# Performance work log

Hardware: AMD Instinct MI355X
Metric: run time of the kernel (lower is better)

The kernel has to match this reference:

```python
import jax, jax.numpy as jnp
import numpy as np

WS = 8      # window size
SS = 4      # shift size
NH = 4      # num heads
EPS = 1e-5
MLP_RATIO = 4


def _win_part(x, ws):
    # x: [B,D,H,W,C] -> [B*nD*nH*nW, ws^3, C]
    B, D, H, W, C = x.shape
    x = x.reshape(B, D // ws, ws, H // ws, ws, W // ws, ws, C)
    x = x.transpose(0, 1, 3, 5, 2, 4, 6, 7)
    return x.reshape(-1, ws * ws * ws, C)


def _win_rev(w, ws, B, D, H, W):
    C = w.shape[-1]
    x = w.reshape(B, D // ws, H // ws, W // ws, ws, ws, ws, C)
    x = x.transpose(0, 1, 4, 2, 5, 3, 6, 7)
    return x.reshape(B, D, H, W, C)


def _ln(x, g, b):
    m = jnp.mean(x, axis=-1, keepdims=True)
    v = jnp.mean((x - m) ** 2, axis=-1, keepdims=True)
    return (x - m) / jnp.sqrt(v + EPS) * g + b


def _rel_index(ws):
    coords = np.stack(np.meshgrid(np.arange(ws), np.arange(ws), np.arange(ws), indexing='ij'))  # [3,ws,ws,ws]
    cf = coords.reshape(3, -1)                      # [3, ws^3]
    rel = (cf[:, :, None] - cf[:, None, :]).transpose(1, 2, 0) + (ws - 1)  # [N,N,3]
    return rel[..., 0] * (2 * ws - 1) ** 2 + rel[..., 1] * (2 * ws - 1) + rel[..., 2]


def _attn_mask(D, H, W, ws, ss):
    img = np.zeros((1, D, H, W, 1), dtype=np.float32)
    cnt = 0
    sl = (slice(0, -ws), slice(-ws, -ss), slice(-ss, None))
    for d in sl:
        for h in sl:
            for w in sl:
                img[:, d, h, w, :] = cnt
                cnt += 1
    mw = np.asarray(_win_part(jnp.asarray(img), ws))[..., 0]  # [nW, ws^3]
    diff = mw[:, None, :] - mw[:, :, None]
    return np.where(diff != 0, -100.0, 0.0).astype(np.float32)


def setup_inputs() -> dict:
    key = jax.random.key(0)
    ks = jax.random.split(key, 12)
    B, D, H, W, C = 1, 16, 64, 64, 128
    mh = MLP_RATIO * C
    s = 0.02
    return {
        'x': jax.random.normal(ks[0], (B, D, H, W, C), jnp.float32),
        'attn_mask': jnp.asarray(_attn_mask(D, H, W, WS, SS)),
        'rel_index': jnp.asarray(_rel_index(WS), jnp.int32),
        'rel_bias': jax.random.normal(ks[1], ((2 * WS - 1) ** 3, NH), jnp.float32) * s,
        'qkv_w': jax.random.normal(ks[2], (3 * C, C), jnp.float32) * s,
        'qkv_b': jnp.zeros((3 * C,), jnp.float32),
        'proj_w': jax.random.normal(ks[3], (C, C), jnp.float32) * s,
        'proj_b': jnp.zeros((C,), jnp.float32),
        'norm1_g': jnp.ones((C,), jnp.float32),
        'norm1_b': jnp.zeros((C,), jnp.float32),
        'norm2_g': jnp.ones((C,), jnp.float32),
        'norm2_b': jnp.zeros((C,), jnp.float32),
        'mlp_w1': jax.random.normal(ks[4], (mh, C), jnp.float32) * s,
        'mlp_b1': jnp.zeros((mh,), jnp.float32),
        'mlp_w2': jax.random.normal(ks[5], (C, mh), jnp.float32) * s,
        'mlp_b2': jnp.zeros((C,), jnp.float32),
    }


def reference(x, attn_mask, rel_index, rel_bias, qkv_w, qkv_b, proj_w, proj_b,
              norm1_g, norm1_b, norm2_g, norm2_b, mlp_w1, mlp_b1, mlp_w2, mlp_b2):
    B, D, H, W, C = x.shape
    ws, ss, nh = WS, SS, NH
    hd = C // nh
    scale = hd ** -0.5
    N = ws ** 3
    shortcut = x
    h = _ln(x, norm1_g, norm1_b)
    h = jnp.roll(h, (-ss, -ss, -ss), axis=(1, 2, 3))
    xw = _win_part(h, ws)                 # [B_, N, C]
    B_ = xw.shape[0]
    nW = attn_mask.shape[0]
    qkv = xw @ qkv_w.T + qkv_b            # [B_, N, 3C]
    qkv = qkv.reshape(B_, N, 3, nh, hd).transpose(2, 0, 3, 1, 4)  # [3,B_,h,N,hd]
    q, k, v = qkv[0] * scale, qkv[1], qkv[2]
    attn = jnp.einsum('bhnd,bhmd->bhnm', q, k)
    rpe = rel_bias[rel_index.reshape(-1)].reshape(N, N, nh).transpose(2, 0, 1)  # [h,N,N]
    attn = attn + rpe[None]
    attn = attn.reshape(B_ // nW, nW, nh, N, N) + attn_mask[None, :, None]
    attn = jax.nn.softmax(attn.reshape(B_, nh, N, N), axis=-1)
    out = jnp.einsum('bhnm,bhmd->bhnd', attn, v).transpose(0, 2, 1, 3).reshape(B_, N, C)
    out = out @ proj_w.T + proj_b
    out = _win_rev(out, ws, B, D, H, W)
    out = jnp.roll(out, (ss, ss, ss), axis=(1, 2, 3))
    x = shortcut + out
    h2 = _ln(x, norm2_g, norm2_b)
    h2 = jax.nn.gelu(h2 @ mlp_w1.T + mlp_b1, approximate=False)
    return x + h2 @ mlp_w2.T + mlp_b2
```

## Files before the change

### kernel.cpp

```cpp
#include <hip/hip_runtime.h>
#include <math.h>

typedef __bf16 bf16;
typedef __bf16 bf16x4 __attribute__((ext_vector_type(4)));
typedef __bf16 bf16x8 __attribute__((ext_vector_type(8)));
typedef float f32x4 __attribute__((ext_vector_type(4)));
typedef unsigned short u16;
typedef u16 u16x2 __attribute__((ext_vector_type(2)));

#define LOG2E 1.4426950408889634f

__device__ __forceinline__ float b2f(u16 b) {
  return (float)__builtin_bit_cast(bf16, b);
}

__global__ void sniff_k(const unsigned* __restrict__ xw_, int* __restrict__ flag) {
  int lane = threadIdx.x;
  int c = 0;
#pragma unroll
  for (int j = 0; j < 4; j++) {
    unsigned e = (xw_[lane * 4 + j] >> 7) & 0xFFu;
    c += (e >= 100u && e <= 140u) ? 1 : 0;
  }
#pragma unroll
  for (int d = 1; d < 64; d <<= 1) c += __shfl_xor(c, d);
  if (lane == 0) *flag = (c >= 150) ? 1 : 0;
}

__global__ __launch_bounds__(256) void canon_big_k(const void* __restrict__ src,
                                                   bf16* __restrict__ dst,
                                                   const int* __restrict__ flag) {
  int i = (blockIdx.x * 256 + threadIdx.x) * 8;
  if (*flag) {
    *(bf16x8*)&dst[i] = *(const bf16x8*)((const bf16*)src + i);
  } else {
    const float* s = (const float*)src + i;
    bf16x8 v;
#pragma unroll
    for (int j = 0; j < 8; j++) v[j] = (bf16)s[j];
    *(bf16x8*)&dst[i] = v;
  }
}

struct CanonArgs {
  const void* src[13];
  bf16* dst[13];
  int n[13];
};

__global__ __launch_bounds__(256) void canon_small_k(CanonArgs a,
                                                     const int* __restrict__ flag) {
  int ti = blockIdx.y;
  int i = blockIdx.x * 256 + threadIdx.x;
  if (i >= a.n[ti]) return;
  if (*flag)
    a.dst[ti][i] = ((const bf16*)a.src[ti])[i];
  else
    a.dst[ti][i] = (bf16)((const float*)a.src[ti])[i];
}

__global__ __launch_bounds__(256) void rpem_k(const int* __restrict__ ridx,
                                              const bf16* __restrict__ rbias,
                                              bf16* __restrict__ rpem) {
  int t = blockIdx.x * 256 + threadIdx.x;
  int m0 = (t & 127) * 4, q = (t >> 7) & 511, h = (t >> 16) & 3, ty = t >> 18;
  int qd = q >> 6, qh = (q >> 3) & 7, qw = q & 7;
  int4 ri = *(const int4*)&ridx[q * 512 + m0];
  const int rv[4] = {ri.x, ri.y, ri.z, ri.w};
  bf16x4 o;
#pragma unroll
  for (int j = 0; j < 4; j++) {
    int m = m0 + j;
    int md = m >> 6, mh = (m >> 3) & 7, mw = m & 7;
    bool diff = ((ty & 4) && ((qd < 4) != (md < 4))) ||
                ((ty & 2) && ((qh < 4) != (mh < 4))) ||
                ((ty & 1) && ((qw < 4) != (mw < 4)));
    float v = (float)rbias[rv[j] * 4 + h] * LOG2E;
    o[j] = (bf16)(v + (diff ? -144.2695041f : 0.f));
  }
  *(bf16x4*)&rpem[(size_t)t * 4] = o;
}

template <int ROLL>
__global__ __launch_bounds__(256) void ln_k(const bf16* __restrict__ x,
                                            const bf16* __restrict__ g,
                                            const bf16* __restrict__ bsh,
                                            bf16* __restrict__ out) {
  int wave = threadIdx.x >> 6, lane = threadIdx.x & 63;
  int tok = blockIdx.x * 4 + wave;
  size_t src;
  if (ROLL) {
    int win = tok >> 9, pos = tok & 511;
    int rd = (win >> 6) * 8 + (pos >> 6);
    int rh = ((win >> 3) & 7) * 8 + ((pos >> 3) & 7);
    int rw = (win & 7) * 8 + (pos & 7);
    int od = (rd + 4) & 15, oh = (rh + 4) & 63, ow = (rw + 4) & 63;
    src = (size_t)((od * 64 + oh) * 64 + ow) * 128;
  } else {
    src = (size_t)tok * 128;
  }
  int ch = lane * 2;
  u16x2 xv = *(const u16x2*)(x + src + ch);
  float f0 = b2f(xv[0]), f1 = b2f(xv[1]);
  float s = f0 + f1, sq = f0 * f0 + f1 * f1;
#pragma unroll
  for (int d = 1; d < 64; d <<= 1) {
    s += __shfl_xor(s, d);
    sq += __shfl_xor(sq, d);
  }
  float mean = s * (1.f / 128.f);
  float var = sq * (1.f / 128.f) - mean * mean;
  float rstd = rsqrtf(fmaxf(var, 0.f) + 1e-5f);
  u16x2 gv = *(const u16x2*)(g + ch), bv = *(const u16x2*)(bsh + ch);
  u16x2 ov;
  ov[0] = __builtin_bit_cast(u16, (bf16)((f0 - mean) * rstd * b2f(gv[0]) + b2f(bv[0])));
  ov[1] = __builtin_bit_cast(u16, (bf16)((f1 - mean) * rstd * b2f(gv[1]) + b2f(bv[1])));
  *(u16x2*)(out + (size_t)tok * 128 + ch) = ov;
}

template <int EPI, int BM, int N_, int K_>
__global__ __launch_bounds__(256) void gemm_k(const bf16* __restrict__ A,
                                              const bf16* __restrict__ B,
                                              const bf16* __restrict__ bias,
                                              void* __restrict__ outv,
                                              const bf16* __restrict__ resid,
                                              const int* __restrict__ flag) {
  __shared__ __align__(16) u16 SM[2][(BM + 128) * 64];
  const int t = threadIdx.x;
  const int wave = t >> 6, lane = t & 63, l15 = lane & 15, quad = lane >> 4;
  const int m0 = blockIdx.x * BM, n0 = blockIdx.y * 128;
  constexpr int MI = BM / 32;
  constexpr int NC = K_ / 64;
  constexpr int PASSES = (BM + 128) / 32;
  int fl = 0;
  if constexpr (EPI == 3) fl = *flag;
  f32x4 acc[MI][4] = {};
  const int wr = (wave >> 1) * (BM / 2), wc = (wave & 1) * 64;
  const int srow = t >> 3;
  const int sc16 = t & 7;

  auto stage = [&](int c, int buf) {
#pragma unroll
    for (int p = 0; p < PASSES; p++) {
      int row = p * 32 + srow;
      int cs = sc16 ^ (row & 7);
      const u16* src;
      if (row < BM)
        src = (const u16*)A + (size_t)(m0 + row) * K_ + c * 64 + cs * 8;
      else
        src = (const u16*)B + (size_t)(n0 + row - BM) * K_ + c * 64 + cs * 8;
      __builtin_amdgcn_global_load_lds(
          (const __attribute__((address_space(1))) void*)src,
          (__attribute__((address_space(3))) void*)&SM[buf][row * 64 + sc16 * 8],
          16, 0, 0);
    }
  };

  stage(0, 0);
  __syncthreads();
#pragma unroll
  for (int c = 0; c < NC; c++) {
    if (c + 1 < NC) stage(c + 1, (c + 1) & 1);
    const char* cur = (const char*)SM[c & 1];
#pragma unroll
    for (int ks = 0; ks < 2; ks++) {
      bf16x8 a[MI], b[4];
#pragma unroll
      for (int i = 0; i < MI; i++) {
        int row = wr + i * 16 + l15;
        a[i] = *(const bf16x8*)(cur + row * 128 +
                                (((ks * 4 + quad) ^ (row & 7)) << 4));
      }
#pragma unroll
      for (int j = 0; j < 4; j++) {
        int row = BM + wc + j * 16 + l15;
        b[j] = *(const bf16x8*)(cur + row * 128 +
                                (((ks * 4 + quad) ^ (row & 7)) << 4));
      }
#pragma unroll
      for (int i = 0; i < MI; i++)
#pragma unroll
        for (int j = 0; j < 4; j++)
          acc[i][j] =
              __builtin_amdgcn_mfma_f32_16x16x32_bf16(a[i], b[j], acc[i][j], 0, 0, 0);
    }
    if (c + 1 < NC) __syncthreads();
  }
  const float qscale = 0.17677669529663687f * LOG2E;
#pragma unroll
  for (int i = 0; i < MI; i++) {
#pragma unroll
    for (int r = 0; r < 4; r++) {
      int tok = m0 + wr + i * 16 + quad * 4 + r;
      size_t obase = 0;
      if constexpr (EPI == 1) {
        int win = tok >> 9, pos = tok & 511;
        int rd = (win >> 6) * 8 + (pos >> 6);
        int rh = ((win >> 3) & 7) * 8 + ((pos >> 3) & 7);
        int rw = (win & 7) * 8 + (pos & 7);
        int od = (rd + 4) & 15, oh = (rh + 4) & 63, ow = (rw + 4) & 63;
        obase = (size_t)((od * 64 + oh) * 64 + ow) * 128;
      } else if constexpr (EPI != 0) {
        obase = (size_t)tok * N_;
      }
#pragma unroll
      for (int j = 0; j < 4; j++) {
        int gn = n0 + wc + j * 16 + l15;
        float v = acc[i][j][r] + (float)bias[gn];
        if constexpr (EPI == 0) {
          int tensor = gn >> 7, c = gn & 127, head = c >> 5, d = c & 31;
          if (tensor == 0) v *= qscale;
          int win = tok >> 9, pos = tok & 511;
          size_t off = ((((size_t)tensor * 4 + head) * 128 + win) * 512 + pos) * 32 + d;
          ((bf16*)outv)[off] = (bf16)v;
        } else if constexpr (EPI == 1) {
          v += (float)resid[obase + gn];
          ((bf16*)outv)[obase + gn] = (bf16)v;
        } else if constexpr (EPI == 2) {
          float v2 = v * v;
          float u2 = v * (2.30220806f + 0.10294323f * v2);
          float e2 = exp2f(u2);
          float rcp = __builtin_amdgcn_rcpf(e2 + 1.f);
          v = v - v * rcp;
          ((bf16*)outv)[obase + gn] = (bf16)v;
        } else {
          v += (float)resid[obase + gn];
          if (fl)
            ((bf16*)outv)[obase + gn] = (bf16)v;
          else
            ((float*)outv)[obase + gn] = v;
        }
      }
    }
  }
}

__global__ __launch_bounds__(512, 4) void attn_k(const bf16* __restrict__ qkv,
                                                 const bf16* __restrict__ rpem,
                                                 bf16* __restrict__ att) {
  __shared__ __align__(16) bf16 sVt[32 * 512];
  __shared__ __align__(16) bf16 sP[8][32 * 64];
  const int t = threadIdx.x;
  const int p = blockIdx.x;
  const int win = ((p >> 6) << 3) | (p & 7);
  const int mid = (p >> 3) & 7;
  const int head = mid >> 1, qh = mid & 1;
  const int wave = t >> 6, lane = t & 63, l15 = lane & 15, quad = lane >> 4;

  const int wd = win >> 6, wh = (win >> 3) & 7, ww = win & 7;
  const int type = ((wd == 1) << 2) | ((wh == 7) << 1) | (ww == 7);

  const size_t hw32 = (size_t)512 * 32;
  const bf16* qp = qkv + ((size_t)(0 * 4 + head) * 128 + win) * hw32;
  const bf16* kp = qkv + ((size_t)(1 * 4 + head) * 128 + win) * hw32;
  const bf16* vp = qkv + ((size_t)(2 * 4 + head) * 128 + win) * hw32;
  const bf16* rpeh = rpem + (size_t)(type * 4 + head) * 512 * 512;
  const int qbase = qh * 256 + wave * 32;

  {
    int kpi = t >> 3, dblk = (t & 7) * 4;
    char* sb = (char*)sVt;
#pragma unroll
    for (int kb = 0; kb < 4; kb++) {
      const bf16* v0 = vp + (size_t)(kb * 128 + 2 * kpi) * 32 + dblk;
      bf16x4 a = *(const bf16x4*)v0;
      bf16x4 b = *(const bf16x4*)(v0 + 32);
      int keyw = kb * 64 + kpi;
#pragma unroll
      for (int dd = 0; dd < 4; dd++) {
        int row = dblk + dd;
        unsigned wv = (unsigned)__builtin_bit_cast(u16, a[dd]) |
                      ((unsigned)__builtin_bit_cast(u16, b[dd]) << 16);
        *(unsigned*)(sb + ((row * 1024 + keyw * 4) ^ ((row & 7) << 4))) = wv;
      }
    }
  }

  bf16x8 qa[2];
#pragma unroll
  for (int nt = 0; nt < 2; nt++)
    qa[nt] = *(const bf16x8*)(qp + (size_t)(qbase + nt * 16 + l15) * 32 + quad * 8);

  bf16x8 ones;
#pragma unroll
  for (int e = 0; e < 8; e++) ones[e] = (bf16)1.0f;

  __syncthreads();

  f32x4 O[2][2] = {};
  f32x4 O2[2] = {};
  char* pw = (char*)sP[wave];
  const char* sv = (const char*)sVt;
  const int swz = (l15 & 7) << 4;

#pragma unroll 1
  for (int kt = 0; kt < 8; kt++) {
    bf16x8 kb[4];
    bf16x4 rv[4][2];
#pragma unroll
    for (int mt = 0; mt < 4; mt++) {
      kb[mt] = *(const bf16x8*)(kp + (size_t)(kt * 64 + mt * 16 + l15) * 32 +
                                quad * 8);
#pragma unroll
      for (int nt = 0; nt < 2; nt++)
        rv[mt][nt] =
            *(const bf16x4*)(rpeh + (size_t)(qbase + nt * 16 + l15) * 512 +
                             kt * 64 + mt * 16 + quad * 4);
    }
    f32x4 S[4][2];
#pragma unroll
    for (int mt = 0; mt < 4; mt++)
#pragma unroll
      for (int nt = 0; nt < 2; nt++) {
        f32x4 c;
#pragma unroll
        for (int r = 0; r < 4; r++) c[r] = (float)rv[mt][nt][r];
        S[mt][nt] = __builtin_amdgcn_mfma_f32_16x16x32_bf16(kb[mt], qa[nt], c, 0, 0, 0);
      }
#pragma unroll
    for (int nt = 0; nt < 2; nt++)
#pragma unroll
      for (int mt = 0; mt < 4; mt++) {
        bf16x4 pv;
#pragma unroll
        for (int r = 0; r < 4; r++) pv[r] = (bf16)exp2f(S[mt][nt][r]);
        *(bf16x4*)(pw + (((nt * 16 + l15) * 128 + mt * 32 + quad * 8) ^ swz)) = pv;
      }
#pragma unroll
    for (int s = 0; s < 2; s++) {
      int vc = kt * 128 + s * 64 + quad * 16;
      int pc = s * 64 + quad * 16;
      bf16x8 va0 = *(const bf16x8*)(sv + ((l15 * 1024 + vc) ^ swz));
      bf16x8 va1 = *(const bf16x8*)(sv + (((16 + l15) * 1024 + vc) ^ swz));
      bf16x8 pb0 = *(const bf16x8*)(pw + ((l15 * 128 + pc) ^ swz));
      bf16x8 pb1 = *(const bf16x8*)(pw + (((16 + l15) * 128 + pc) ^ swz));
      O[0][0] = __builtin_amdgcn_mfma_f32_16x16x32_bf16(va0, pb0, O[0][0], 0, 0, 0);
      O[0][1] = __builtin_amdgcn_mfma_f32_16x16x32_bf16(va0, pb1, O[0][1], 0, 0, 0);
      O[1][0] = __builtin_amdgcn_mfma_f32_16x16x32_bf16(va1, pb0, O[1][0], 0, 0, 0);
      O[1][1] = __builtin_amdgcn_mfma_f32_16x16x32_bf16(va1, pb1, O[1][1], 0, 0, 0);
      O2[0] = __builtin_amdgcn_mfma_f32_16x16x32_bf16(ones, pb0, O2[0], 0, 0, 0);
      O2[1] = __builtin_amdgcn_mfma_f32_16x16x32_bf16(ones, pb1, O2[1], 0, 0, 0);
    }
  }
#pragma unroll
  for (int nt = 0; nt < 2; nt++) {
    float inv = __builtin_amdgcn_rcpf(O2[nt][0]);
    int q = qbase + nt * 16 + l15;
#pragma unroll
    for (int dm = 0; dm < 2; dm++) {
      bf16x4 o;
#pragma unroll
      for (int r = 0; r < 4; r++) o[r] = (bf16)(O[dm][nt][r] * inv);
      *(bf16x4*)(att + ((size_t)win * 512 + q) * 128 + head * 32 + dm * 16 +
                 quad * 4) = o;
    }
  }
}

extern "C" void kernel_launch(void* const* d_in, const int* in_sizes, int n_in,
                              void* d_out, int out_size, void* d_ws,
                              size_t ws_size, hipStream_t stream) {
  const int* rel_index = (const int*)d_in[2];
  char* w = (char*)d_ws;

  int* flag = (int*)w;
  bf16* rb_c = (bf16*)(w + (64ull << 10));
  bf16* qw_c = (bf16*)(w + (128ull << 10));
  bf16* pw_c = (bf16*)(w + (256ull << 10));
  bf16* w1_c = (bf16*)(w + (320ull << 10));
  bf16* w2_c = (bf16*)(w + (512ull << 10));
  bf16* qb_c = (bf16*)(w + (704ull << 10));
  bf16* pb_c = (bf16*)(w + (708ull << 10));
  bf16* g1_c = (bf16*)(w + (712ull << 10));
  bf16* b1n_c = (bf16*)(w + (716ull << 10));
  bf16* g2_c = (bf16*)(w + (720ull << 10));
  bf16* b2n_c = (bf16*)(w + (724ull << 10));
  bf16* mb1_c = (bf16*)(w + (728ull << 10));
  bf16* mb2_c = (bf16*)(w + (732ull << 10));
  bf16* x_c = (bf16*)(w + (1ull << 20));
  bf16* xw = (bf16*)(w + (17ull << 20));
  bf16* qkvb = (bf16*)(w + (33ull << 20));
  bf16* x2 = (bf16*)(w + (99ull << 20));
  bf16* rpem = x2;
  bf16* att = xw;
  bf16* h2 = xw;
  bf16* a1 = qkvb;

  sniff_k<<<1, 64, 0, stream>>>((const unsigned*)d_in[0], flag);
  canon_big_k<<<4096, 256, 0, stream>>>(d_in[0], x_c, flag);

  CanonArgs ca;
  const int srcidx[13] = {3, 4, 5, 6, 7, 8, 9, 10, 11, 12, 13, 14, 15};
  bf16* dsts[13] = {rb_c, qw_c, qb_c, pw_c, pb_c, g1_c, b1n_c,
                    g2_c, b2n_c, w1_c, mb1_c, w2_c, mb2_c};
  for (int i = 0; i < 13; i++) {
    ca.src[i] = d_in[srcidx[i]];
    ca.dst[i] = dsts[i];
    ca.n[i] = in_sizes[srcidx[i]];
  }
  canon_small_k<<<dim3(256, 13), 256, 0, stream>>>(ca, flag);

  rpem_k<<<8192, 256, 0, stream>>>(rel_index, rb_c, rpem);
  ln_k<1><<<16384, 256, 0, stream>>>(x_c, g1_c, b1n_c, xw);
  gemm_k<0, 128, 384, 128><<<dim3(512, 3), 256, 0, stream>>>(xw, qw_c, qb_c,
                                                             qkvb, nullptr, flag);
  attn_k<<<1024, 512, 0, stream>>>(qkvb, rpem, att);
  gemm_k<1, 64, 128, 128><<<dim3(1024, 1), 256, 0, stream>>>(att, pw_c, pb_c,
                                                             x2, x_c, flag);
  ln_k<0><<<16384, 256, 0, stream>>>(x2, g2_c, b2n_c, h2);
  gemm_k<2, 128, 512, 128><<<dim3(512, 4), 256, 0, stream>>>(h2, w1_c, mb1_c,
                                                             a1, nullptr, flag);
  gemm_k<3, 64, 128, 512><<<dim3(1024, 1), 256, 0, stream>>>(a1, w2_c, mb2_c,
                                                             d_out, x2, flag);
}
```

Baseline: 414.6 us.

## Fuse input conversion into LN/proj, reorder rpe layout, retune GEMM tiles

Removes the separate full-tensor fp32-to-bf16 conversion kernel: the first LayerNorm and the projection residual read the raw input directly, branching on the dtype flag. The rpe+mask table is written in a layout matching the attention kernel's MFMA accumulator order, so attention loads it with wide 16-byte vector loads. The GEMM gains a BK template parameter: most GEMMs stage the whole K=128 in one buffer, and the M tiles shrink to 64 rows for more blocks. This trades lower conversion traffic and fewer launches for smaller tiles with less data reuse.

```diff
diff --git a/kernel.cpp b/kernel.cpp
--- a/kernel.cpp
+++ b/kernel.cpp
@@ -25,21 +25,6 @@
 #pragma unroll
   for (int d = 1; d < 64; d <<= 1) c += __shfl_xor(c, d);
   if (lane == 0) *flag = (c >= 150) ? 1 : 0;
-}
-
-__global__ __launch_bounds__(256) void canon_big_k(const void* __restrict__ src,
-                                                   bf16* __restrict__ dst,
-                                                   const int* __restrict__ flag) {
-  int i = (blockIdx.x * 256 + threadIdx.x) * 8;
-  if (*flag) {
-    *(bf16x8*)&dst[i] = *(const bf16x8*)((const bf16*)src + i);
-  } else {
-    const float* s = (const float*)src + i;
-    bf16x8 v;
-#pragma unroll
-    for (int j = 0; j < 8; j++) v[j] = (bf16)s[j];
-    *(bf16x8*)&dst[i] = v;
-  }
 }
 
 struct CanonArgs {
@@ -65,6 +50,7 @@
   int t = blockIdx.x * 256 + threadIdx.x;
   int m0 = (t & 127) * 4, q = (t >> 7) & 511, h = (t >> 16) & 3, ty = t >> 18;
   int qd = q >> 6, qh = (q >> 3) & 7, qw = q & 7;
+  int kt = m0 >> 6, mt = (m0 >> 4) & 3, quad = (m0 >> 2) & 3;
   int4 ri = *(const int4*)&ridx[q * 512 + m0];
   const int rv[4] = {ri.x, ri.y, ri.z, ri.w};
   bf16x4 o;
@@ -78,14 +64,17 @@
     float v = (float)rbias[rv[j] * 4 + h] * LOG2E;
     o[j] = (bf16)(v + (diff ? -144.2695041f : 0.f));
   }
-  *(bf16x4*)&rpem[(size_t)t * 4] = o;
+  size_t out = ((size_t)(ty * 4 + h) << 18) +
+               (((size_t)(kt * 4 + quad) * 512 + q) * 16 + mt * 4);
+  *(bf16x4*)&rpem[out] = o;
 }
 
 template <int ROLL>
-__global__ __launch_bounds__(256) void ln_k(const bf16* __restrict__ x,
+__global__ __launch_bounds__(256) void ln_k(const void* __restrict__ xin,
                                             const bf16* __restrict__ g,
                                             const bf16* __restrict__ bsh,
-                                            bf16* __restrict__ out) {
+                                            bf16* __restrict__ out,
+                                            const int* __restrict__ flag) {
   int wave = threadIdx.x >> 6, lane = threadIdx.x & 63;
   int tok = blockIdx.x * 4 + wave;
   size_t src;
@@ -100,8 +89,16 @@
     src = (size_t)tok * 128;
   }
   int ch = lane * 2;
-  u16x2 xv = *(const u16x2*)(x + src + ch);
-  float f0 = b2f(xv[0]), f1 = b2f(xv[1]);
+  float f0, f1;
+  if (ROLL && !*flag) {
+    const float* xf = (const float*)xin + src + ch;
+    f0 = xf[0];
+    f1 = xf[1];
+  } else {
+    u16x2 xv = *(const u16x2*)((const bf16*)xin + src + ch);
+    f0 = b2f(xv[0]);
+    f1 = b2f(xv[1]);
+  }
   float s = f0 + f1, sq = f0 * f0 + f1 * f1;
 #pragma unroll
   for (int d = 1; d < 64; d <<= 1) {
@@ -118,40 +115,42 @@
   *(u16x2*)(out + (size_t)tok * 128 + ch) = ov;
 }
 
-template <int EPI, int BM, int N_, int K_>
+template <int EPI, int BM, int BK, int N_, int K_>
 __global__ __launch_bounds__(256) void gemm_k(const bf16* __restrict__ A,
                                               const bf16* __restrict__ B,
                                               const bf16* __restrict__ bias,
                                               void* __restrict__ outv,
-                                              const bf16* __restrict__ resid,
+                                              const void* __restrict__ residv,
                                               const int* __restrict__ flag) {
-  __shared__ __align__(16) u16 SM[2][(BM + 128) * 64];
+  constexpr int NC = K_ / BK;
+  constexpr int NBUF = (NC > 1) ? 2 : 1;
+  __shared__ __align__(16) u16 SM[NBUF][(BM + 128) * BK];
   const int t = threadIdx.x;
   const int wave = t >> 6, lane = t & 63, l15 = lane & 15, quad = lane >> 4;
   const int m0 = blockIdx.x * BM, n0 = blockIdx.y * 128;
   constexpr int MI = BM / 32;
-  constexpr int NC = K_ / 64;
-  constexpr int PASSES = (BM + 128) / 32;
   int fl = 0;
-  if constexpr (EPI == 3) fl = *flag;
+  if constexpr (EPI == 1 || EPI == 3) fl = *flag;
   f32x4 acc[MI][4] = {};
   const int wr = (wave >> 1) * (BM / 2), wc = (wave & 1) * 64;
-  const int srow = t >> 3;
-  const int sc16 = t & 7;
+  constexpr int TPR = BK / 8;
+  constexpr int RPP = 256 / TPR;
+  constexpr int PASSES = (BM + 128) / RPP;
+  const int srow = t / TPR, sc16 = t % TPR;
 
   auto stage = [&](int c, int buf) {
 #pragma unroll
     for (int p = 0; p < PASSES; p++) {
-      int row = p * 32 + srow;
+      int row = p * RPP + srow;
       int cs = sc16 ^ (row & 7);
       const u16* src;
       if (row < BM)
-        src = (const u16*)A + (size_t)(m0 + row) * K_ + c * 64 + cs * 8;
+        src = (const u16*)A + (size_t)(m0 + row) * K_ + c * BK + cs * 8;
       else
-        src = (const u16*)B + (size_t)(n0 + row - BM) * K_ + c * 64 + cs * 8;
+        src = (const u16*)B + (size_t)(n0 + row - BM) * K_ + c * BK + cs * 8;
       __builtin_amdgcn_global_load_lds(
           (const __attribute__((address_space(1))) void*)src,
-          (__attribute__((address_space(3))) void*)&SM[buf][row * 64 + sc16 * 8],
+          (__attribute__((address_space(3))) void*)&SM[buf][row * BK + sc16 * 8],
           16, 0, 0);
     }
   };
@@ -163,18 +162,18 @@
     if (c + 1 < NC) stage(c + 1, (c + 1) & 1);
     const char* cur = (const char*)SM[c & 1];
 #pragma unroll
-    for (int ks = 0; ks < 2; ks++) {
+    for (int ks = 0; ks < BK / 32; ks++) {
       bf16x8 a[MI], b[4];
 #pragma unroll
       for (int i = 0; i < MI; i++) {
         int row = wr + i * 16 + l15;
-        a[i] = *(const bf16x8*)(cur + row * 128 +
+        a[i] = *(const bf16x8*)(cur + row * (BK * 2) +
                                 (((ks * 4 + quad) ^ (row & 7)) << 4));
       }
 #pragma unroll
       for (int j = 0; j < 4; j++) {
         int row = BM + wc + j * 16 + l15;
-        b[j] = *(const bf16x8*)(cur + row * 128 +
+        b[j] = *(const bf16x8*)(cur + row * (BK * 2) +
                                 (((ks * 4 + quad) ^ (row & 7)) << 4));
       }
 #pragma unroll
@@ -214,7 +213,9 @@
           size_t off = ((((size_t)tensor * 4 + head) * 128 + win) * 512 + pos) * 32 + d;
           ((bf16*)outv)[off] = (bf16)v;
         } else if constexpr (EPI == 1) {
-          v += (float)resid[obase + gn];
+          float rs = fl ? (float)((const bf16*)residv)[obase + gn]
+                        : ((const float*)residv)[obase + gn];
+          v += rs;
           ((bf16*)outv)[obase + gn] = (bf16)v;
         } else if constexpr (EPI == 2) {
           float v2 = v * v;
@@ -224,7 +225,7 @@
           v = v - v * rcp;
           ((bf16*)outv)[obase + gn] = (bf16)v;
         } else {
-          v += (float)resid[obase + gn];
+          v += (float)((const bf16*)residv)[obase + gn];
           if (fl)
             ((bf16*)outv)[obase + gn] = (bf16)v;
           else
@@ -254,7 +255,7 @@
   const bf16* qp = qkv + ((size_t)(0 * 4 + head) * 128 + win) * hw32;
   const bf16* kp = qkv + ((size_t)(1 * 4 + head) * 128 + win) * hw32;
   const bf16* vp = qkv + ((size_t)(2 * 4 + head) * 128 + win) * hw32;
-  const bf16* rpeh = rpem + (size_t)(type * 4 + head) * 512 * 512;
+  const bf16* rpeh = rpem + ((size_t)(type * 4 + head) << 18);
   const int qbase = qh * 256 + wave * 32;
 
   {
@@ -296,16 +297,17 @@
 #pragma unroll 1
   for (int kt = 0; kt < 8; kt++) {
     bf16x8 kb[4];
-    bf16x4 rv[4][2];
-#pragma unroll
-    for (int mt = 0; mt < 4; mt++) {
+    bf16x8 rv8[2][2];
+#pragma unroll
+    for (int mt = 0; mt < 4; mt++)
       kb[mt] = *(const bf16x8*)(kp + (size_t)(kt * 64 + mt * 16 + l15) * 32 +
                                 quad * 8);
 #pragma unroll
-      for (int nt = 0; nt < 2; nt++)
-        rv[mt][nt] =
-            *(const bf16x4*)(rpeh + (size_t)(qbase + nt * 16 + l15) * 512 +
-                             kt * 64 + mt * 16 + quad * 4);
+    for (int nt = 0; nt < 2; nt++) {
+      const bf16* rb =
+          rpeh + ((size_t)(kt * 4 + quad) * 512 + (qbase + nt * 16 + l15)) * 16;
+      rv8[nt][0] = *(const bf16x8*)rb;
+      rv8[nt][1] = *(const bf16x8*)(rb + 8);
     }
     f32x4 S[4][2];
 #pragma unroll
@@ -314,7 +316,7 @@
       for (int nt = 0; nt < 2; nt++) {
         f32x4 c;
 #pragma unroll
-        for (int r = 0; r < 4; r++) c[r] = (float)rv[mt][nt][r];
+        for (int r = 0; r < 4; r++) c[r] = (float)rv8[nt][mt >> 1][(mt & 1) * 4 + r];
         S[mt][nt] = __builtin_amdgcn_mfma_f32_16x16x32_bf16(kb[mt], qa[nt], c, 0, 0, 0);
       }
 #pragma unroll
@@ -377,7 +379,6 @@
   bf16* b2n_c = (bf16*)(w + (724ull << 10));
   bf16* mb1_c = (bf16*)(w + (728ull << 10));
   bf16* mb2_c = (bf16*)(w + (732ull << 10));
-  bf16* x_c = (bf16*)(w + (1ull << 20));
   bf16* xw = (bf16*)(w + (17ull << 20));
   bf16* qkvb = (bf16*)(w + (33ull << 20));
   bf16* x2 = (bf16*)(w + (99ull << 20));
@@ -387,7 +388,6 @@
   bf16* a1 = qkvb;
 
   sniff_k<<<1, 64, 0, stream>>>((const unsigned*)d_in[0], flag);
-  canon_big_k<<<4096, 256, 0, stream>>>(d_in[0], x_c, flag);
 
   CanonArgs ca;
   const int srcidx[13] = {3, 4, 5, 6, 7, 8, 9, 10, 11, 12, 13, 14, 15};
@@ -401,15 +401,15 @@
   canon_small_k<<<dim3(256, 13), 256, 0, stream>>>(ca, flag);
 
   rpem_k<<<8192, 256, 0, stream>>>(rel_index, rb_c, rpem);
-  ln_k<1><<<16384, 256, 0, stream>>>(x_c, g1_c, b1n_c, xw);
-  gemm_k<0, 128, 384, 128><<<dim3(512, 3), 256, 0, stream>>>(xw, qw_c, qb_c,
-                                                             qkvb, nullptr, flag);
+  ln_k<1><<<16384, 256, 0, stream>>>(d_in[0], g1_c, b1n_c, xw, flag);
+  gemm_k<0, 64, 128, 384, 128><<<dim3(1024, 3), 256, 0, stream>>>(
+      xw, qw_c, qb_c, qkvb, nullptr, flag);
   attn_k<<<1024, 512, 0, stream>>>(qkvb, rpem, att);
-  gemm_k<1, 64, 128, 128><<<dim3(1024, 1), 256, 0, stream>>>(att, pw_c, pb_c,
-                                                             x2, x_c, flag);
-  ln_k<0><<<16384, 256, 0, stream>>>(x2, g2_c, b2n_c, h2);
-  gemm_k<2, 128, 512, 128><<<dim3(512, 4), 256, 0, stream>>>(h2, w1_c, mb1_c,
-                                                             a1, nullptr, flag);
-  gemm_k<3, 64, 128, 512><<<dim3(1024, 1), 256, 0, stream>>>(a1, w2_c, mb2_c,
-                                                             d_out, x2, flag);
-}
+  gemm_k<1, 64, 128, 128, 128><<<dim3(1024, 1), 256, 0, stream>>>(
+      att, pw_c, pb_c, x2, d_in[0], flag);
+  ln_k<0><<<16384, 256, 0, stream>>>(x2, g2_c, b2n_c, h2, flag);
+  gemm_k<2, 64, 128, 512, 128><<<dim3(1024, 4), 256, 0, stream>>>(
+      h2, w1_c, mb1_c, a1, nullptr, flag);
+  gemm_k<3, 64, 64, 128, 512><<<dim3(1024, 1), 256, 0, stream>>>(
+      a1, w2_c, mb2_c, d_out, x2, flag);
+}
```

Result: faster. 390.1 us (-5.9%).
